# Performance work log

Measured on AMD Instinct MI355X. Metric: run time of the kernel, lower is better.

The kernel has to match this reference:

```python
import jax, jax.numpy as jnp
import numpy as np

G, N, E, F, H, O, MO = 64, 2048, 16384, 128, 128, 128, 128


def setup_inputs() -> dict:
    key = jax.random.key(0)
    ks = jax.random.split(key, 12)
    # edges: per-graph contiguous blocks, local indices in [0, N-2] (never touch center N-1)
    src_l = jax.random.randint(ks[0], (G, E), 0, N - 1)
    dst_l = jax.random.randint(ks[1], (G, E), 0, N - 1)
    offs = (jnp.arange(G, dtype=jnp.int64) * N)[:, None]
    edge_index = jnp.stack([(src_l + offs).reshape(-1), (dst_l + offs).reshape(-1)]).astype(jnp.int64)
    x = jax.random.normal(ks[2], (G * N, F), dtype=jnp.float32)
    batch = jnp.repeat(jnp.arange(G, dtype=jnp.int64), N)
    center_node_indices = jnp.full((G,), N - 1, dtype=jnp.int64)
    def lin(k, fan_in, shape):
        return jax.random.normal(k, shape, dtype=jnp.float32) / np.sqrt(fan_in)
    return {
        "x": x, "edge_index": edge_index, "batch": batch,
        "center_node_indices": center_node_indices,
        "W1": lin(ks[3], F, (F, H)), "b1": jnp.zeros((H,), jnp.float32),
        "W2": lin(ks[4], F, (F, O)), "b2": jnp.zeros((O,), jnp.float32),
        "W3": lin(ks[5], F, (F, O)), "b3": jnp.zeros((O,), jnp.float32),
        "Wm": lin(ks[6], H + F, (H + F, MO)), "bm": jnp.zeros((MO,), jnp.float32),
    }


def _gcn(x, src, dst, W, b):
    # PyG GCNConv: D^{-1/2}(A+I)D^{-1/2} X W + b, messages src->dst, deg at dst
    n = x.shape[0]
    h = x @ W
    deg = 1.0 + jax.ops.segment_sum(jnp.ones(src.shape[0], h.dtype), dst, num_segments=n)
    dis = jax.lax.rsqrt(deg)
    msg = h[src] * (dis[src] * dis[dst])[:, None]
    agg = jax.ops.segment_sum(msg, dst, num_segments=n)
    return agg + h * (1.0 / deg)[:, None] + b


_gcn_v = jax.vmap(_gcn, in_axes=(0, 0, 0, None, None))


def reference(x, edge_index, batch, center_node_indices, W1, b1, W2, b2, W3, b3, Wm, bm):
    g = center_node_indices.shape[0]
    n = x.shape[0] // g
    e = edge_index.shape[1] // g
    offs = (jnp.arange(g) * n)[:, None]
    src = edge_index[0].reshape(g, e) - offs  # local per-graph edges
    dst = edge_index[1].reshape(g, e) - offs
    xg = x.reshape(g, n, -1)                      # [G,N,F]
    h1 = _gcn_v(xg, src, dst, W1, b1)             # [G,N,H]
    ce = h1[jnp.arange(g), center_node_indices]   # [G,H] center embeddings
    x_nc = xg[:, : n - 1]                         # non-center nodes (center = N-1)
    hd = W1.shape[1]
    # MLP(cat([center_emb, node_feat])) = relu(ce@Wm_top + x@Wm_bot + bm)
    mask = jax.nn.relu((ce @ Wm[:hd])[:, None, :] + x_nc @ Wm[hd:] + bm)  # [G,N-1,MO]
    core = _gcn_v(mask * x_nc, src, dst, W2, b2)          # [G,N-1,O]
    red = _gcn_v((1.0 - mask) * x_nc, src, dst, W3, b3)   # [G,N-1,O]
    return core.mean(axis=0), red.mean(axis=0)
```

## Files before the change

### kernel.cpp

```cpp
#include <hip/hip_runtime.h>

typedef unsigned short u16;
typedef unsigned int uint32;
typedef __bf16 bf16x8 __attribute__((ext_vector_type(8)));
typedef float f32x4 __attribute__((ext_vector_type(4)));

static constexpr int Gg = 64;
static constexpr int Nn = 2048;
static constexpr int Ee = 16384;
static constexpr int GN = Gg * Nn;
static constexpr int GE = Gg * Ee;

__device__ __forceinline__ u16 f2u(float f) {
    uint32 i = __float_as_uint(f);
    uint32 r = (i + 0x7FFFu + ((i >> 16) & 1u)) >> 16;
    return (u16)r;
}
__device__ __forceinline__ float lo16f(uint32 v) { return __uint_as_float(v << 16); }
__device__ __forceinline__ float hi16f(uint32 v) { return __uint_as_float(v & 0xffff0000u); }


__global__ __launch_bounds__(1024) void k_hist(const int* __restrict__ ei, int* __restrict__ deg,
                                               float* __restrict__ dis, float* __restrict__ invdeg) {
    int g = blockIdx.x, t = threadIdx.x;
    __shared__ int h[2048];
    h[t] = 0; h[t + 1024] = 0;
    __syncthreads();
    #pragma unroll
    for (int k = 0; k < 16; ++k) {
        int d = ei[GE + g * Ee + k * 1024 + t];
        atomicAdd(&h[d & (Nn - 1)], 1);
    }
    __syncthreads();
    #pragma unroll
    for (int k = 0; k < 2; ++k) {
        int i = k * 1024 + t;
        int c = h[i];
        deg[(g << 11) + i] = c;
        float dd = 1.0f + (float)c;
        dis[(g << 11) + i] = rsqrtf(dd);
        invdeg[(g << 11) + i] = 1.0f / dd;
    }
}

__global__ __launch_bounds__(1024) void k_scan_g(const int* __restrict__ deg, int* __restrict__ rp) {
    int g = blockIdx.x, t = threadIdx.x;
    int i0 = 2 * t, i1 = 2 * t + 1;
    int c0 = deg[(g << 11) + i0];
    int c1 = deg[(g << 11) + i1];
    __shared__ int ps[1024];
    ps[t] = c0 + c1; __syncthreads();
    for (int off = 1; off < 1024; off <<= 1) {
        int v = (t >= off) ? ps[t - off] : 0;
        __syncthreads();
        ps[t] += v;
        __syncthreads();
    }
    int base = g * Ee + ps[t] - (c0 + c1);
    rp[(g << 11) + i0] = base;
    rp[(g << 11) + i1] = base + c0;
}

__global__ __launch_bounds__(1024) void k_scatter(const int* __restrict__ ei, const float* __restrict__ dis,
                                                  const int* __restrict__ rp, int2* __restrict__ nme) {
    int g = blockIdx.x, t = threadIdx.x;
    __shared__ int curs[2048];
    curs[t] = rp[(g << 11) + t];
    curs[t + 1024] = rp[(g << 11) + t + 1024];
    __syncthreads();
    #pragma unroll
    for (int k = 0; k < 16; ++k) {
        int e = g * Ee + k * 1024 + t;
        int s = ei[e];
        int d = ei[GE + e];
        int p = atomicAdd(&curs[d & (Nn - 1)], 1);
        nme[p] = make_int2(s, __float_as_int(dis[s] * dis[d]));
    }
}

__global__ void k_trans(const float* __restrict__ Wm, u16* __restrict__ Wtp) {
    int tid = blockIdx.x * 256 + threadIdx.x;
    int j = tid & 7, l = (tid >> 3) & 63, kc = tid >> 9;
    int ks = kc >> 3, ct = kc & 7, lm = l & 15, lq = l >> 4;
    int f = ks * 32 + lq * 8 + j, c = ct * 16 + lm;
    Wtp[tid] = f2u(Wm[(128 + f) * 128 + c]);
}

__global__ void k_A(const float* __restrict__ x, const int* __restrict__ center,
                    const float* __restrict__ invdeg, const int* __restrict__ rp,
                    const int* __restrict__ degc, const int2* __restrict__ nme,
                    const float* __restrict__ W1, const float* __restrict__ b1,
                    const float* __restrict__ Wm, const float* __restrict__ bm,
                    float* __restrict__ A) {
    int g = blockIdx.x, t = threadIdx.x;
    __shared__ float cepre[128], ce[128];
    int cg = (g << 11) + center[g];
    float v = x[cg * 128 + t] * invdeg[cg];
    int p0 = rp[cg], p1 = p0 + degc[cg];
    for (int e = p0; e < p1; ++e) {
        int2 m = nme[e];
        v += __int_as_float(m.y) * x[m.x * 128 + t];
    }
    cepre[t] = v; __syncthreads();
    float a = b1[t];
    #pragma unroll 8
    for (int f = 0; f < 128; ++f) a += cepre[f] * W1[f * 128 + t];
    ce[t] = a; __syncthreads();
    float o = bm[t];
    #pragma unroll 8
    for (int h = 0; h < 128; ++h) o += ce[h] * Wm[h * 128 + t];
    A[g * 128 + t] = o;
}

__global__ __launch_bounds__(256) void k_masky(const float* __restrict__ x,
                                               const u16* __restrict__ Wtp,
                                               const float* __restrict__ A,
                                               u16* __restrict__ xy) {
    __shared__ float sA[128];
    int t = threadIdx.x;
    int tile = blockIdx.x;
    int g = tile >> 5;
    if (t < 128) sA[t] = A[g * 128 + t];
    __syncthreads();

    int w = t >> 6, l = t & 63;
    int lm = l & 15, lq = l >> 4;
    int row = tile * 64 + w * 16 + lm;
    const float* xrow = x + row * 128;
    const bf16x8* Ap = (const bf16x8*)Wtp;

    float4 xf[8];
    #pragma unroll
    for (int ks = 0; ks < 4; ++ks) {
        xf[2 * ks]     = *(const float4*)(xrow + ks * 32 + lq * 8);
        xf[2 * ks + 1] = *(const float4*)(xrow + ks * 32 + lq * 8 + 4);
    }
    union { u16 u[8]; bf16x8 v; } bf[4];
    #pragma unroll
    for (int ks = 0; ks < 4; ++ks) {
        float4 x0 = xf[2 * ks], x1 = xf[2 * ks + 1];
        bf[ks].u[0] = f2u(x0.x); bf[ks].u[1] = f2u(x0.y);
        bf[ks].u[2] = f2u(x0.z); bf[ks].u[3] = f2u(x0.w);
        bf[ks].u[4] = f2u(x1.x); bf[ks].u[5] = f2u(x1.y);
        bf[ks].u[6] = f2u(x1.z); bf[ks].u[7] = f2u(x1.w);
    }

    f32x4 acc[8] = {};
    #pragma unroll
    for (int ks = 0; ks < 4; ++ks) {
        #pragma unroll
        for (int ct = 0; ct < 8; ++ct) {
            bf16x8 a = Ap[(ks * 8 + ct) * 64 + l];
            acc[ct] = __builtin_amdgcn_mfma_f32_16x16x32_bf16(a, bf[ks].v, acc[ct], 0, 0, 0);
        }
    }

    u16* orow = xy + row * 256;
    #pragma unroll
    for (int ct = 0; ct < 8; ++ct) {
        int ch = ct * 16 + lq * 4;
        float4 xv = *(const float4*)(xrow + ch);
        float y0 = fmaxf(acc[ct][0] + sA[ch + 0], 0.f) * xv.x;
        float y1 = fmaxf(acc[ct][1] + sA[ch + 1], 0.f) * xv.y;
        float y2 = fmaxf(acc[ct][2] + sA[ch + 2], 0.f) * xv.z;
        float y3 = fmaxf(acc[ct][3] + sA[ch + 3], 0.f) * xv.w;
        uint4 q;
        q.x = (uint32)f2u(y0)   | ((uint32)f2u(y1)   << 16);
        q.y = (uint32)f2u(xv.x) | ((uint32)f2u(xv.y) << 16);
        q.z = (uint32)f2u(y2)   | ((uint32)f2u(y3)   << 16);
        q.w = (uint32)f2u(xv.z) | ((uint32)f2u(xv.w) << 16);
        *(uint4*)(orow + ct * 32 + lq * 8) = q;
    }
}

#define ACC8(v, cf)                                                     \
    aY0 += (cf) * lo16f((v).x); aY1 += (cf) * hi16f((v).x);             \
    aX0 += (cf) * lo16f((v).y); aX1 += (cf) * hi16f((v).y);             \
    aY2 += (cf) * lo16f((v).z); aY3 += (cf) * hi16f((v).z);             \
    aX2 += (cf) * lo16f((v).w); aX3 += (cf) * hi16f((v).w);

__global__ __launch_bounds__(256) void k_propx(const u16* __restrict__ xy,
                                               const float* __restrict__ invdeg,
                                               const int* __restrict__ rp,
                                               const int* __restrict__ degc,
                                               const int2* __restrict__ nme,
                                               float* __restrict__ zp) {
    int b = blockIdx.x;
    int p = b & 7, c = b >> 3;
    int t = threadIdx.x, w = t >> 6, l = t & 63;
    int half = l >> 5, cl = l & 31;
    int i = c * 4 + w;
    float aY0 = 0.f, aY1 = 0.f, aY2 = 0.f, aY3 = 0.f;
    float aX0 = 0.f, aX1 = 0.f, aX2 = 0.f, aX3 = 0.f;

    for (int g8 = 0; g8 < 8; ++g8) {
        int gid = ((p * 8 + g8) << 11) + i;
        if (half == 0) {
            float cf = invdeg[gid];
            uint4 v = *(const uint4*)(xy + (size_t)gid * 256 + cl * 8);
            ACC8(v, cf)
        }
        int j = rp[gid], jend = j + degc[gid];
        for (; j + 7 < jend; j += 8) {
            int2 m0 = nme[j + half];
            int2 m1 = nme[j + 2 + half];
            int2 m2 = nme[j + 4 + half];
            int2 m3 = nme[j + 6 + half];
            uint4 v0 = *(const uint4*)(xy + (size_t)m0.x * 256 + cl * 8);
            uint4 v1 = *(const uint4*)(xy + (size_t)m1.x * 256 + cl * 8);
            uint4 v2 = *(const uint4*)(xy + (size_t)m2.x * 256 + cl * 8);
            uint4 v3 = *(const uint4*)(xy + (size_t)m3.x * 256 + cl * 8);
            float c0 = __int_as_float(m0.y), c1 = __int_as_float(m1.y);
            float c2 = __int_as_float(m2.y), c3 = __int_as_float(m3.y);
            ACC8(v0, c0) ACC8(v1, c1) ACC8(v2, c2) ACC8(v3, c3)
        }
        for (; j + 3 < jend; j += 4) {
            int2 m0 = nme[j + half];
            int2 m1 = nme[j + 2 + half];
            uint4 v0 = *(const uint4*)(xy + (size_t)m0.x * 256 + cl * 8);
            uint4 v1 = *(const uint4*)(xy + (size_t)m1.x * 256 + cl * 8);
            float c0 = __int_as_float(m0.y), c1 = __int_as_float(m1.y);
            ACC8(v0, c0) ACC8(v1, c1)
        }
        for (; j < jend; j += 2) {
            int idx = j + half;
            if (idx < jend) {
                int2 m = nme[idx];
                uint4 v = *(const uint4*)(xy + (size_t)m.x * 256 + cl * 8);
                float cf = __int_as_float(m.y);
                ACC8(v, cf)
            }
        }
    }

    aY0 += __shfl_xor(aY0, 32, 64); aY1 += __shfl_xor(aY1, 32, 64);
    aX0 += __shfl_xor(aX0, 32, 64); aX1 += __shfl_xor(aX1, 32, 64);
    aY2 += __shfl_xor(aY2, 32, 64); aY3 += __shfl_xor(aY3, 32, 64);
    aX2 += __shfl_xor(aX2, 32, 64); aX3 += __shfl_xor(aX3, 32, 64);
    if (half == 0) {
        float* zr = zp + ((size_t)((p << 11) + i) << 8) + cl * 8;
        *(float4*)(zr) = make_float4(aY0, aY1, aX0, aX1);
        *(float4*)(zr + 4) = make_float4(aY2, aY3, aX2, aX3);
    }
}

__global__ __launch_bounds__(256) void k_reduce(const float* __restrict__ zp,
                                                const float* __restrict__ W2, const float* __restrict__ b2,
                                                const float* __restrict__ W3, const float* __restrict__ b3,
                                                float* __restrict__ out) {
    int i = blockIdx.x;
    int t = threadIdx.x;
    __shared__ float zm[128], zxm[128];
    float s = 0.f;
    #pragma unroll
    for (int p = 0; p < 8; ++p) s += zp[((size_t)((p << 11) + i) << 8) + t];
    s *= (1.0f / 64.0f);
    int k = t >> 2, r = t & 3;
    if (r < 2) zm[2 * k + r] = s; else zxm[2 * k + (r - 2)] = s;
    __syncthreads();
    int cc = t & 127;
    if (t < 128) {
        float acc = b2[cc];
        #pragma unroll 8
        for (int f = 0; f < 128; ++f) acc += zm[f] * W2[f * 128 + cc];
        out[i * 128 + cc] = acc;
    } else {
        float acc = b3[cc];
        #pragma unroll 8
        for (int f = 0; f < 128; ++f) acc += (zxm[f] - zm[f]) * W3[f * 128 + cc];
        out[2047 * 128 + i * 128 + cc] = acc;
    }
}


extern "C" void kernel_launch(void* const* d_in, const int* in_sizes, int n_in,
                              void* d_out, int out_size, void* d_ws, size_t ws_size,
                              hipStream_t stream) {
    const float* x    = (const float*)d_in[0];
    const int* ei     = (const int*)d_in[1];
    const int* center = (const int*)d_in[3];
    const float* W1 = (const float*)d_in[4];
    const float* b1 = (const float*)d_in[5];
    const float* W2 = (const float*)d_in[6];
    const float* b2 = (const float*)d_in[7];
    const float* W3 = (const float*)d_in[8];
    const float* b3 = (const float*)d_in[9];
    const float* Wm = (const float*)d_in[10];
    const float* bm = (const float*)d_in[11];
    float* out = (float*)d_out;

    char* ws = (char*)d_ws;
    int*   degc   = (int*)(ws + 0);
    float* dis    = (float*)(ws + 524288);
    float* invdeg = (float*)(ws + 1048576);
    int*   rp     = (int*)(ws + 1572864);
    float* A      = (float*)(ws + 2097152);
    u16*   Wtp    = (u16*)(ws + 2129920);
    int2*  nme    = (int2*)(ws + 2162688);
    float* zp     = (float*)(ws + 10551296);
    u16*   xy     = (u16*)(ws + 27328512);

    k_hist<<<dim3(Gg), dim3(1024), 0, stream>>>(ei, degc, dis, invdeg);
    k_scan_g<<<dim3(Gg), dim3(1024), 0, stream>>>(degc, rp);
    k_scatter<<<dim3(Gg), dim3(1024), 0, stream>>>(ei, dis, rp, nme);
    k_trans<<<dim3(64), dim3(256), 0, stream>>>(Wm, Wtp);
    k_A<<<dim3(Gg), dim3(128), 0, stream>>>(x, center, invdeg, rp, degc, nme, W1, b1, Wm, bm, A);
    k_masky<<<dim3(2048), dim3(256), 0, stream>>>(x, Wtp, A, xy);
    k_propx<<<dim3(4096), dim3(256), 0, stream>>>(xy, invdeg, rp, degc, nme, zp);
    k_reduce<<<dim3(Nn - 1), dim3(256), 0, stream>>>(zp, W2, b2, W3, b3, out);
}
```

Before: 258.8 us.

## Fuse CSR build into one kernel and software-pipeline edge loads in propagation

Merges the histogram, scan and scatter kernels into a single per-graph kernel. Degrees, rsqrt norms and cursors stay in shared memory, which removes two launches and the global round-trips for deg and dis. Row ends now come from rp[i+1] via a sentinel instead of a separate degree array. The propagation kernel preloads all row bounds and prefetches the next batch of edge records while gathering the current rows, so index-load latency overlaps with the gathers. It also drops the 4-wide remainder loop, which leaves more work in the 2-wide tail loop.

After: 281.1 us. +8.6%, slower.

```diff
diff --git a/kernel.cpp b/kernel.cpp
--- a/kernel.cpp
+++ b/kernel.cpp
@@ -19,11 +19,14 @@
 __device__ __forceinline__ float lo16f(uint32 v) { return __uint_as_float(v << 16); }
 __device__ __forceinline__ float hi16f(uint32 v) { return __uint_as_float(v & 0xffff0000u); }
 
-
-__global__ __launch_bounds__(1024) void k_hist(const int* __restrict__ ei, int* __restrict__ deg,
-                                               float* __restrict__ dis, float* __restrict__ invdeg) {
+__global__ __launch_bounds__(1024) void k_build(const int* __restrict__ ei,
+                                                float* __restrict__ invdeg,
+                                                int* __restrict__ rp, int2* __restrict__ nme) {
     int g = blockIdx.x, t = threadIdx.x;
     __shared__ int h[2048];
+    __shared__ float sdis[2048];
+    __shared__ int ps[1024];
+    int* curs = h;
     h[t] = 0; h[t + 1024] = 0;
     __syncthreads();
     #pragma unroll
@@ -32,23 +35,14 @@
         atomicAdd(&h[d & (Nn - 1)], 1);
     }
     __syncthreads();
-    #pragma unroll
-    for (int k = 0; k < 2; ++k) {
-        int i = k * 1024 + t;
-        int c = h[i];
-        deg[(g << 11) + i] = c;
-        float dd = 1.0f + (float)c;
-        dis[(g << 11) + i] = rsqrtf(dd);
-        invdeg[(g << 11) + i] = 1.0f / dd;
-    }
-}
-
-__global__ __launch_bounds__(1024) void k_scan_g(const int* __restrict__ deg, int* __restrict__ rp) {
-    int g = blockIdx.x, t = threadIdx.x;
-    int i0 = 2 * t, i1 = 2 * t + 1;
-    int c0 = deg[(g << 11) + i0];
-    int c1 = deg[(g << 11) + i1];
-    __shared__ int ps[1024];
+    int c0 = h[2 * t], c1 = h[2 * t + 1];
+    {
+        float d0 = 1.0f + (float)c0, d1 = 1.0f + (float)c1;
+        sdis[2 * t] = rsqrtf(d0);
+        sdis[2 * t + 1] = rsqrtf(d1);
+        invdeg[(g << 11) + 2 * t] = 1.0f / d0;
+        invdeg[(g << 11) + 2 * t + 1] = 1.0f / d1;
+    }
     ps[t] = c0 + c1; __syncthreads();
     for (int off = 1; off < 1024; off <<= 1) {
         int v = (t >= off) ? ps[t - off] : 0;
@@ -57,24 +51,19 @@
         __syncthreads();
     }
     int base = g * Ee + ps[t] - (c0 + c1);
-    rp[(g << 11) + i0] = base;
-    rp[(g << 11) + i1] = base + c0;
-}
-
-__global__ __launch_bounds__(1024) void k_scatter(const int* __restrict__ ei, const float* __restrict__ dis,
-                                                  const int* __restrict__ rp, int2* __restrict__ nme) {
-    int g = blockIdx.x, t = threadIdx.x;
-    __shared__ int curs[2048];
-    curs[t] = rp[(g << 11) + t];
-    curs[t + 1024] = rp[(g << 11) + t + 1024];
+    rp[(g << 11) + 2 * t] = base;
+    rp[(g << 11) + 2 * t + 1] = base + c0;
+    if (g == 63 && t == 1023) rp[GN] = GE;
+    curs[2 * t] = base;
+    curs[2 * t + 1] = base + c0;
     __syncthreads();
     #pragma unroll
     for (int k = 0; k < 16; ++k) {
         int e = g * Ee + k * 1024 + t;
         int s = ei[e];
         int d = ei[GE + e];
-        int p = atomicAdd(&curs[d & (Nn - 1)], 1);
-        nme[p] = make_int2(s, __float_as_int(dis[s] * dis[d]));
+        int pos = atomicAdd(&curs[d & (Nn - 1)], 1);
+        nme[pos] = make_int2(s, __float_as_int(sdis[s & (Nn - 1)] * sdis[d & (Nn - 1)]));
     }
 }
 
@@ -88,7 +77,7 @@
 
 __global__ void k_A(const float* __restrict__ x, const int* __restrict__ center,
                     const float* __restrict__ invdeg, const int* __restrict__ rp,
-                    const int* __restrict__ degc, const int2* __restrict__ nme,
+                    const int2* __restrict__ nme,
                     const float* __restrict__ W1, const float* __restrict__ b1,
                     const float* __restrict__ Wm, const float* __restrict__ bm,
                     float* __restrict__ A) {
@@ -96,7 +85,7 @@
     __shared__ float cepre[128], ce[128];
     int cg = (g << 11) + center[g];
     float v = x[cg * 128 + t] * invdeg[cg];
-    int p0 = rp[cg], p1 = p0 + degc[cg];
+    int p0 = rp[cg], p1 = rp[cg + 1];
     for (int e = p0; e < p1; ++e) {
         int2 m = nme[e];
         v += __int_as_float(m.y) * x[m.x * 128 + t];
@@ -182,7 +171,6 @@
 __global__ __launch_bounds__(256) void k_propx(const u16* __restrict__ xy,
                                                const float* __restrict__ invdeg,
                                                const int* __restrict__ rp,
-                                               const int* __restrict__ degc,
                                                const int2* __restrict__ nme,
                                                float* __restrict__ zp) {
     int b = blockIdx.x;
@@ -193,6 +181,14 @@
     float aY0 = 0.f, aY1 = 0.f, aY2 = 0.f, aY3 = 0.f;
     float aX0 = 0.f, aX1 = 0.f, aX2 = 0.f, aX3 = 0.f;
 
+    int jb[8], je[8];
+    #pragma unroll
+    for (int g8 = 0; g8 < 8; ++g8) {
+        int gid = ((p * 8 + g8) << 11) + i;
+        jb[g8] = rp[gid];
+        je[g8] = rp[gid + 1];
+    }
+
     for (int g8 = 0; g8 < 8; ++g8) {
         int gid = ((p * 8 + g8) << 11) + i;
         if (half == 0) {
@@ -200,27 +196,30 @@
             uint4 v = *(const uint4*)(xy + (size_t)gid * 256 + cl * 8);
             ACC8(v, cf)
         }
-        int j = rp[gid], jend = j + degc[gid];
-        for (; j + 7 < jend; j += 8) {
-            int2 m0 = nme[j + half];
-            int2 m1 = nme[j + 2 + half];
-            int2 m2 = nme[j + 4 + half];
-            int2 m3 = nme[j + 6 + half];
-            uint4 v0 = *(const uint4*)(xy + (size_t)m0.x * 256 + cl * 8);
-            uint4 v1 = *(const uint4*)(xy + (size_t)m1.x * 256 + cl * 8);
-            uint4 v2 = *(const uint4*)(xy + (size_t)m2.x * 256 + cl * 8);
-            uint4 v3 = *(const uint4*)(xy + (size_t)m3.x * 256 + cl * 8);
-            float c0 = __int_as_float(m0.y), c1 = __int_as_float(m1.y);
-            float c2 = __int_as_float(m2.y), c3 = __int_as_float(m3.y);
+        int j = jb[g8], jend = je[g8];
+        int2 n0, n1, n2, n3;
+        bool have = (j + 7 < jend);
+        if (have) {
+            n0 = nme[j + half];     n1 = nme[j + 2 + half];
+            n2 = nme[j + 4 + half]; n3 = nme[j + 6 + half];
+        }
+        while (have) {
+            int jn = j + 8;
+            bool nxt = (jn + 7 < jend);
+            uint4 v0 = *(const uint4*)(xy + (size_t)n0.x * 256 + cl * 8);
+            uint4 v1 = *(const uint4*)(xy + (size_t)n1.x * 256 + cl * 8);
+            uint4 v2 = *(const uint4*)(xy + (size_t)n2.x * 256 + cl * 8);
+            uint4 v3 = *(const uint4*)(xy + (size_t)n3.x * 256 + cl * 8);
+            int2 m0, m1, m2, m3;
+            if (nxt) {
+                m0 = nme[jn + half];     m1 = nme[jn + 2 + half];
+                m2 = nme[jn + 4 + half]; m3 = nme[jn + 6 + half];
+            }
+            float c0 = __int_as_float(n0.y), c1 = __int_as_float(n1.y);
+            float c2 = __int_as_float(n2.y), c3 = __int_as_float(n3.y);
             ACC8(v0, c0) ACC8(v1, c1) ACC8(v2, c2) ACC8(v3, c3)
-        }
-        for (; j + 3 < jend; j += 4) {
-            int2 m0 = nme[j + half];
-            int2 m1 = nme[j + 2 + half];
-            uint4 v0 = *(const uint4*)(xy + (size_t)m0.x * 256 + cl * 8);
-            uint4 v1 = *(const uint4*)(xy + (size_t)m1.x * 256 + cl * 8);
-            float c0 = __int_as_float(m0.y), c1 = __int_as_float(m1.y);
-            ACC8(v0, c0) ACC8(v1, c1)
+            n0 = m0; n1 = m1; n2 = m2; n3 = m3;
+            j = jn; have = nxt;
         }
         for (; j < jend; j += 2) {
             int idx = j + half;
@@ -290,22 +289,18 @@
     float* out = (float*)d_out;
 
     char* ws = (char*)d_ws;
-    int*   degc   = (int*)(ws + 0);
-    float* dis    = (float*)(ws + 524288);
-    float* invdeg = (float*)(ws + 1048576);
-    int*   rp     = (int*)(ws + 1572864);
-    float* A      = (float*)(ws + 2097152);
-    u16*   Wtp    = (u16*)(ws + 2129920);
-    int2*  nme    = (int2*)(ws + 2162688);
-    float* zp     = (float*)(ws + 10551296);
-    u16*   xy     = (u16*)(ws + 27328512);
-
-    k_hist<<<dim3(Gg), dim3(1024), 0, stream>>>(ei, degc, dis, invdeg);
-    k_scan_g<<<dim3(Gg), dim3(1024), 0, stream>>>(degc, rp);
-    k_scatter<<<dim3(Gg), dim3(1024), 0, stream>>>(ei, dis, rp, nme);
+    float* invdeg = (float*)(ws + 0);
+    int*   rp     = (int*)(ws + 524288);
+    float* A      = (float*)(ws + 1052672);
+    u16*   Wtp    = (u16*)(ws + 1085440);
+    int2*  nme    = (int2*)(ws + 1118208);
+    float* zp     = (float*)(ws + 9506816);
+    u16*   xy     = (u16*)(ws + 26283776);
+
+    k_build<<<dim3(Gg), dim3(1024), 0, stream>>>(ei, invdeg, rp, nme);
     k_trans<<<dim3(64), dim3(256), 0, stream>>>(Wm, Wtp);
-    k_A<<<dim3(Gg), dim3(128), 0, stream>>>(x, center, invdeg, rp, degc, nme, W1, b1, Wm, bm, A);
+    k_A<<<dim3(Gg), dim3(128), 0, stream>>>(x, center, invdeg, rp, nme, W1, b1, Wm, bm, A);
     k_masky<<<dim3(2048), dim3(256), 0, stream>>>(x, Wtp, A, xy);
-    k_propx<<<dim3(4096), dim3(256), 0, stream>>>(xy, invdeg, rp, degc, nme, zp);
+    k_propx<<<dim3(4096), dim3(256), 0, stream>>>(xy, invdeg, rp, nme, zp);
     k_reduce<<<dim3(Nn - 1), dim3(256), 0, stream>>>(zp, W2, b2, W3, b3, out);
 }
```
